# Kernel optimization log

Hardware: AMD Instinct MI355X
Metric: run time of the kernel (lower is better)

## Reference

```python
import jax, jax.numpy as jnp
import numpy as np

IN_CH = 512
OUT_CH = 3
W_DIM = 512
CLAMP = 256.0

# setup_filter([1,3,3,1]): outer product, normalized to sum 1 (separable FIR)
_f1 = np.array([1.0, 3.0, 3.0, 1.0], dtype=np.float32)
_f2 = np.outer(_f1, _f1)
_f2 = _f2 / _f2.sum()
FIR = jnp.asarray(_f2)  # [4,4], symmetric so flipping is a no-op


def setup_inputs() -> dict:
    key = jax.random.key(0)
    ks = jax.random.split(key, 5)
    return {
        "x": jax.random.normal(ks[0], (8, IN_CH, 128, 128), jnp.float32),
        "w": jax.random.normal(ks[1], (8, W_DIM), jnp.float32),
        "skip": jax.random.normal(ks[2], (8, OUT_CH, 64, 64), jnp.float32),
        "affine_w": jax.random.normal(ks[3], (IN_CH, W_DIM), jnp.float32),
        "affine_b": jnp.ones((IN_CH,), jnp.float32),  # bias_init=1
        "weight": jax.random.normal(ks[4], (OUT_CH, IN_CH, 1, 1), jnp.float32),
        "bias": jnp.zeros((OUT_CH,), jnp.float32),
    }


def _upsample2d(s):
    # upfirdn2d.upsample2d(up=2): zero-insert, pad, FIR filter, gain = up**2 = 4.
    # lax lhs_dilation=2 gives 2H-1 samples (no trailing zero); torch ref pads
    # (2,1) on the 2H-length sequence -> equivalent lax padding is (2,2).
    C = s.shape[1]
    k = jnp.tile((FIR * 4.0)[None, None], (C, 1, 1, 1))  # [C,1,4,4] depthwise
    return jax.lax.conv_general_dilated(
        s, k, window_strides=(1, 1), padding=((2, 2), (2, 2)),
        lhs_dilation=(2, 2),
        dimension_numbers=("NCHW", "OIHW", "NCHW"),
        feature_group_count=C,
    )


def reference(x, w, skip, affine_w, affine_b, weight, bias):
    # affine DenseLayer: default activation='lrelu' (alpha=0.2, gain=sqrt(2))
    affine_gain = 1.0 / np.sqrt(W_DIM)
    styles = jax.nn.leaky_relu(w @ (affine_w * affine_gain).T + affine_b, 0.2)
    styles = styles * np.float32(np.sqrt(2.0))  # [B, IN_CH]

    # modulated 1x1 conv, demodulate=False, groups=batch ->
    # out[b,o,h,w] = sum_i (weight[o,i]*wg) * styles[b,i] * x[b,i,h,w]
    wm = weight[:, :, 0, 0] * (1.0 / IN_CH)  # weight_gain = 1/in_channels
    y = jnp.einsum("oi,bi,bihw->bohw", wm, styles, x)

    # bias_act: linear act + clamp
    y = jnp.clip(y + bias[None, :, None, None], -CLAMP, CLAMP)

    return y + _upsample2d(skip)
```

## Files before the change

kernel.cpp:

```cpp
#include <hip/hip_runtime.h>
#include <math.h>


#define IN_CH 512
#define OUT_CH 3
#define NPIX 16384
#define NB 8

__global__ __launch_bounds__(256) void coeff_kernel(
    const float* __restrict__ w, const float* __restrict__ aw,
    const float* __restrict__ ab, const float* __restrict__ wt,
    float* __restrict__ coeff) {
  const int b  = blockIdx.x >> 4;
  const int rg = blockIdx.x & 15;
  const int tid = threadIdx.x;
  __shared__ float wv[512];
  wv[tid]       = w[b * 512 + tid];
  wv[tid + 256] = w[b * 512 + 256 + tid];
  __syncthreads();
  const int wave = tid >> 6, lane = tid & 63;
  const float gain = 1.0f / sqrtf(512.0f);
  #pragma unroll 2
  for (int r = 0; r < 8; ++r) {
    const int i = rg * 32 + wave * 8 + r;
    const float* row = aw + (size_t)i * 512;
    float s = 0.f;
    #pragma unroll
    for (int k = 0; k < 8; ++k) s += row[lane + 64 * k] * wv[lane + 64 * k];
    #pragma unroll
    for (int off = 32; off >= 1; off >>= 1) s += __shfl_xor(s, off, 64);
    if (lane == 0) {
      float v = s * gain + ab[i];
      v = (v > 0.f ? v : 0.2f * v) * 1.41421356237f;
      #pragma unroll
      for (int o = 0; o < OUT_CH; ++o)
        coeff[b * (OUT_CH * IN_CH) + o * IN_CH + i] =
            wt[o * IN_CH + i] * (1.0f / 512.0f) * v;
    }
  }
}

__global__ __launch_bounds__(256) void main_kernel(
    const float* __restrict__ x, const float* __restrict__ coeff,
    const float* __restrict__ bias, const float* __restrict__ skip,
    float* __restrict__ out) {
  const int b   = blockIdx.x >> 8;
  const int g   = blockIdx.x & 255;
  const int p0  = g * 64;
  const int tid = threadIdx.x;
  const int col   = tid & 15;
  const int split = tid >> 4;

  __shared__ float lds_c[16 * 100];
  for (int idx = tid; idx < 1600; idx += 256) {
    int s = idx / 100, r = idx - s * 100;
    if (r < 96) {
      int k = r / 3, o = r - 3 * k;
      lds_c[idx] = coeff[b * (OUT_CH * IN_CH) + o * IN_CH + s * 32 + k];
    }
  }
  __syncthreads();

  const float* xp = x + ((size_t)(b * IN_CH + split * 32)) * NPIX + p0 + col * 4;
  const float* cp = lds_c + split * 100;

  float acc[12];
  #pragma unroll
  for (int j = 0; j < 12; ++j) acc[j] = 0.f;

  #pragma unroll 8
  for (int k = 0; k < 32; ++k) {
    float4 xv = *reinterpret_cast<const float4*>(xp);
    xp += NPIX;
    float c0 = cp[k * 3 + 0], c1 = cp[k * 3 + 1], c2 = cp[k * 3 + 2];
    acc[0] += c0 * xv.x; acc[1]  += c0 * xv.y; acc[2]  += c0 * xv.z; acc[3]  += c0 * xv.w;
    acc[4] += c1 * xv.x; acc[5]  += c1 * xv.y; acc[6]  += c1 * xv.z; acc[7]  += c1 * xv.w;
    acc[8] += c2 * xv.x; acc[9]  += c2 * xv.y; acc[10] += c2 * xv.z; acc[11] += c2 * xv.w;
  }

  __shared__ float red[16][16][13];
  #pragma unroll
  for (int j = 0; j < 12; ++j) red[split][col][j] = acc[j];
  __syncthreads();
  #pragma unroll
  for (int s = 8; s >= 1; s >>= 1) {
    if (split < s) {
      #pragma unroll
      for (int j = 0; j < 12; ++j) red[split][col][j] += red[split + s][col][j];
    }
    __syncthreads();
  }

  if (tid < 192) {
    const int o = tid >> 6;
    const int l = tid & 63;
    const int p = p0 + l;
    float v = red[0][l >> 2][o * 4 + (l & 3)] + bias[o];
    v = fminf(fmaxf(v, -256.f), 256.f);

    const int yy = p >> 7, xx = p & 127;
    int iy0, ix0; float wy0, wy1, wx0, wx1;
    if (yy & 1) { iy0 = (yy - 1) >> 1; wy0 = 3.f; wy1 = 1.f; }
    else        { iy0 = (yy >> 1) - 1; wy0 = 1.f; wy1 = 3.f; }
    if (xx & 1) { ix0 = (xx - 1) >> 1; wx0 = 3.f; wx1 = 1.f; }
    else        { ix0 = (xx >> 1) - 1; wx0 = 1.f; wx1 = 3.f; }

    const float* sp = skip + ((size_t)(b * OUT_CH + o)) * 4096;
    float s00 = (iy0 >= 0     && ix0 >= 0    ) ? sp[iy0 * 64 + ix0]           : 0.f;
    float s01 = (iy0 >= 0     && ix0 + 1 < 64) ? sp[iy0 * 64 + ix0 + 1]       : 0.f;
    float s10 = (iy0 + 1 < 64 && ix0 >= 0    ) ? sp[(iy0 + 1) * 64 + ix0]     : 0.f;
    float s11 = (iy0 + 1 < 64 && ix0 + 1 < 64) ? sp[(iy0 + 1) * 64 + ix0 + 1] : 0.f;
    float up = (wy0 * (wx0 * s00 + wx1 * s01) + wy1 * (wx0 * s10 + wx1 * s11)) * (1.f / 16.f);

    out[((size_t)(b * OUT_CH + o)) * NPIX + p] = v + up;
  }
}

extern "C" void kernel_launch(void* const* d_in, const int* in_sizes, int n_in,
                              void* d_out, int out_size, void* d_ws, size_t ws_size,
                              hipStream_t stream) {
  const float* x        = (const float*)d_in[0];
  const float* w        = (const float*)d_in[1];
  const float* skip     = (const float*)d_in[2];
  const float* affine_w = (const float*)d_in[3];
  const float* affine_b = (const float*)d_in[4];
  const float* weight   = (const float*)d_in[5];
  const float* bias     = (const float*)d_in[6];
  float* out   = (float*)d_out;
  float* coeff = (float*)d_ws;

  coeff_kernel<<<128, 256, 0, stream>>>(w, affine_w, affine_b, weight, coeff);
  main_kernel<<<NB * 256, 256, 0, stream>>>(x, coeff, bias, skip, out);
}
```

Before: 58.33 us.

## Use wave shuffles for split-K reduction, prefetch skip upsample, widen coeff grid

The main kernel's shared-memory tree reduction, which needed four barriers, is replaced by xor-shuffles inside each wavefront plus one shared-memory pass that sums the four wave partials. The skip-upsample gather is issued before the main loop so its global loads overlap the coefficient staging. Coefficients are padded to stride 4 so each iteration reads them with one float4 LDS load. The coeff kernel gets four times as many blocks, each handling fewer rows, to spread its matrix-vector work across more compute units. The costs are slightly more LDS for the coefficients and extra registers held live for the prefetched upsample value.

```diff
diff --git a/kernel.cpp b/kernel.cpp
--- a/kernel.cpp
+++ b/kernel.cpp
@@ -11,8 +11,8 @@
     const float* __restrict__ w, const float* __restrict__ aw,
     const float* __restrict__ ab, const float* __restrict__ wt,
     float* __restrict__ coeff) {
-  const int b  = blockIdx.x >> 4;
-  const int rg = blockIdx.x & 15;
+  const int b  = blockIdx.x >> 6;
+  const int rg = blockIdx.x & 63;
   const int tid = threadIdx.x;
   __shared__ float wv[512];
   wv[tid]       = w[b * 512 + tid];
@@ -20,9 +20,9 @@
   __syncthreads();
   const int wave = tid >> 6, lane = tid & 63;
   const float gain = 1.0f / sqrtf(512.0f);
-  #pragma unroll 2
-  for (int r = 0; r < 8; ++r) {
-    const int i = rg * 32 + wave * 8 + r;
+  #pragma unroll
+  for (int r = 0; r < 2; ++r) {
+    const int i = rg * 8 + wave * 2 + r;
     const float* row = aw + (size_t)i * 512;
     float s = 0.f;
     #pragma unroll
@@ -51,18 +51,37 @@
   const int col   = tid & 15;
   const int split = tid >> 4;
 
-  __shared__ float lds_c[16 * 100];
-  for (int idx = tid; idx < 1600; idx += 256) {
-    int s = idx / 100, r = idx - s * 100;
-    if (r < 96) {
-      int k = r / 3, o = r - 3 * k;
-      lds_c[idx] = coeff[b * (OUT_CH * IN_CH) + o * IN_CH + s * 32 + k];
-    }
+  __shared__ float lds_c[16 * 32 * 4];
+  for (int idx = tid; idx < 2048; idx += 256) {
+    const int s = idx >> 7, rem = idx & 127, k = rem >> 2, o = rem & 3;
+    lds_c[idx] = (o < 3)
+        ? coeff[b * (OUT_CH * IN_CH) + o * IN_CH + s * 32 + k]
+        : 0.f;
   }
+
+  float up = 0.f;
+  if (tid < 192) {
+    const int o = tid >> 6;
+    const int l = tid & 63;
+    const int p = p0 + l;
+    const int yy = p >> 7, xx = p & 127;
+    int iy0, ix0; float wy0, wy1, wx0, wx1;
+    if (yy & 1) { iy0 = (yy - 1) >> 1; wy0 = 3.f; wy1 = 1.f; }
+    else        { iy0 = (yy >> 1) - 1; wy0 = 1.f; wy1 = 3.f; }
+    if (xx & 1) { ix0 = (xx - 1) >> 1; wx0 = 3.f; wx1 = 1.f; }
+    else        { ix0 = (xx >> 1) - 1; wx0 = 1.f; wx1 = 3.f; }
+    const float* sp = skip + ((size_t)(b * OUT_CH + o)) * 4096;
+    float s00 = (iy0 >= 0     && ix0 >= 0    ) ? sp[iy0 * 64 + ix0]           : 0.f;
+    float s01 = (iy0 >= 0     && ix0 + 1 < 64) ? sp[iy0 * 64 + ix0 + 1]       : 0.f;
+    float s10 = (iy0 + 1 < 64 && ix0 >= 0    ) ? sp[(iy0 + 1) * 64 + ix0]     : 0.f;
+    float s11 = (iy0 + 1 < 64 && ix0 + 1 < 64) ? sp[(iy0 + 1) * 64 + ix0 + 1] : 0.f;
+    up = (wy0 * (wx0 * s00 + wx1 * s01) + wy1 * (wx0 * s10 + wx1 * s11)) * (1.f / 16.f);
+  }
+
   __syncthreads();
 
   const float* xp = x + ((size_t)(b * IN_CH + split * 32)) * NPIX + p0 + col * 4;
-  const float* cp = lds_c + split * 100;
+  const float* cp = lds_c + split * 128;
 
   float acc[12];
   #pragma unroll
@@ -70,49 +89,33 @@
 
   #pragma unroll 8
   for (int k = 0; k < 32; ++k) {
-    float4 xv = *reinterpret_cast<const float4*>(xp);
-    xp += NPIX;
-    float c0 = cp[k * 3 + 0], c1 = cp[k * 3 + 1], c2 = cp[k * 3 + 2];
-    acc[0] += c0 * xv.x; acc[1]  += c0 * xv.y; acc[2]  += c0 * xv.z; acc[3]  += c0 * xv.w;
-    acc[4] += c1 * xv.x; acc[5]  += c1 * xv.y; acc[6]  += c1 * xv.z; acc[7]  += c1 * xv.w;
-    acc[8] += c2 * xv.x; acc[9]  += c2 * xv.y; acc[10] += c2 * xv.z; acc[11] += c2 * xv.w;
+    float4 xv = *reinterpret_cast<const float4*>(xp + (size_t)k * NPIX);
+    float4 c4 = *reinterpret_cast<const float4*>(cp + k * 4);
+    acc[0] += c4.x * xv.x; acc[1]  += c4.x * xv.y; acc[2]  += c4.x * xv.z; acc[3]  += c4.x * xv.w;
+    acc[4] += c4.y * xv.x; acc[5]  += c4.y * xv.y; acc[6]  += c4.y * xv.z; acc[7]  += c4.y * xv.w;
+    acc[8] += c4.z * xv.x; acc[9]  += c4.z * xv.y; acc[10] += c4.z * xv.z; acc[11] += c4.z * xv.w;
   }
 
-  __shared__ float red[16][16][13];
   #pragma unroll
-  for (int j = 0; j < 12; ++j) red[split][col][j] = acc[j];
+  for (int j = 0; j < 12; ++j) {
+    acc[j] += __shfl_xor(acc[j], 16, 64);
+    acc[j] += __shfl_xor(acc[j], 32, 64);
+  }
+  __shared__ float red[4][16][13];
+  const int wave = tid >> 6, lane = tid & 63;
+  if (lane < 16) {
+    #pragma unroll
+    for (int j = 0; j < 12; ++j) red[wave][lane][j] = acc[j];
+  }
   __syncthreads();
-  #pragma unroll
-  for (int s = 8; s >= 1; s >>= 1) {
-    if (split < s) {
-      #pragma unroll
-      for (int j = 0; j < 12; ++j) red[split][col][j] += red[split + s][col][j];
-    }
-    __syncthreads();
-  }
 
   if (tid < 192) {
     const int o = tid >> 6;
     const int l = tid & 63;
-    const int p = p0 + l;
-    float v = red[0][l >> 2][o * 4 + (l & 3)] + bias[o];
+    const int c = l >> 2, j = o * 4 + (l & 3);
+    float v = red[0][c][j] + red[1][c][j] + red[2][c][j] + red[3][c][j] + bias[o];
     v = fminf(fmaxf(v, -256.f), 256.f);
-
-    const int yy = p >> 7, xx = p & 127;
-    int iy0, ix0; float wy0, wy1, wx0, wx1;
-    if (yy & 1) { iy0 = (yy - 1) >> 1; wy0 = 3.f; wy1 = 1.f; }
-    else        { iy0 = (yy >> 1) - 1; wy0 = 1.f; wy1 = 3.f; }
-    if (xx & 1) { ix0 = (xx - 1) >> 1; wx0 = 3.f; wx1 = 1.f; }
-    else        { ix0 = (xx >> 1) - 1; wx0 = 1.f; wx1 = 3.f; }
-
-    const float* sp = skip + ((size_t)(b * OUT_CH + o)) * 4096;
-    float s00 = (iy0 >= 0     && ix0 >= 0    ) ? sp[iy0 * 64 + ix0]           : 0.f;
-    float s01 = (iy0 >= 0     && ix0 + 1 < 64) ? sp[iy0 * 64 + ix0 + 1]       : 0.f;
-    float s10 = (iy0 + 1 < 64 && ix0 >= 0    ) ? sp[(iy0 + 1) * 64 + ix0]     : 0.f;
-    float s11 = (iy0 + 1 < 64 && ix0 + 1 < 64) ? sp[(iy0 + 1) * 64 + ix0 + 1] : 0.f;
-    float up = (wy0 * (wx0 * s00 + wx1 * s01) + wy1 * (wx0 * s10 + wx1 * s11)) * (1.f / 16.f);
-
-    out[((size_t)(b * OUT_CH + o)) * NPIX + p] = v + up;
+    out[((size_t)(b * OUT_CH + o)) * NPIX + p0 + l] = v + up;
   }
 }
 
@@ -129,6 +132,6 @@
   float* out   = (float*)d_out;
   float* coeff = (float*)d_ws;
 
-  coeff_kernel<<<128, 256, 0, stream>>>(w, affine_w, affine_b, weight, coeff);
+  coeff_kernel<<<512, 256, 0, stream>>>(w, affine_w, affine_b, weight, coeff);
   main_kernel<<<NB * 256, 256, 0, stream>>>(x, coeff, bias, skip, out);
 }
```

Result: faster. 53.61 us (-8.1%).
